# Kernel tuning notes

Hardware: AMD Instinct MI355X
Metric: run time of the kernel (lower is better)

The kernel has to match this reference:

```python
import jax, jax.numpy as jnp
import numpy as np

B, C, H, W = 4, 512, 64, 64
CQ = C // 8  # 64 channels for each of query/key projections


def conv1x1(t, w, b):
    # t: [B, Cin, H, W], w: [Cout, Cin], b: [Cout]
    return jnp.einsum('bchw,oc->bohw', t, w) + b[None, :, None, None]


def setup_inputs() -> dict:
    key = jax.random.key(0)
    ks = jax.random.split(key, 12)
    s = 0.05
    return {
        'x':   jax.random.normal(ks[0], (B, C, H, W), jnp.float32),
        'dep': jax.random.normal(ks[1], (B, C, H, W), jnp.float32),
        'wq':  jax.random.normal(ks[2], (CQ, C), jnp.float32) * s,
        'bq':  jnp.zeros((CQ,), jnp.float32),
        'wqd': jax.random.normal(ks[3], (CQ, C), jnp.float32) * s,
        'bqd': jnp.zeros((CQ,), jnp.float32),
        'wk':  jax.random.normal(ks[4], (CQ, C), jnp.float32) * s,
        'bk':  jnp.zeros((CQ,), jnp.float32),
        'wkd': jax.random.normal(ks[5], (CQ, C), jnp.float32) * s,
        'bkd': jnp.zeros((CQ,), jnp.float32),
        'wv':  jax.random.normal(ks[6], (C, C), jnp.float32) * s,
        'bv':  jnp.zeros((C,), jnp.float32),
        'gamma': jnp.full((1,), 0.5, jnp.float32),
    }


def reference(x, dep, wq, bq, wqd, bqd, wk, bk, wkd, bkd, wv, bv, gamma):
    b, c, h, w = x.shape
    n = h * w
    # concatenated RGB+depth query/key projections: [B, 2*CQ, N]
    q = jnp.concatenate([conv1x1(x, wq, bq), conv1x1(dep, wqd, bqd)], axis=1).reshape(b, -1, n)
    k = jnp.concatenate([conv1x1(x, wk, bk), conv1x1(dep, wkd, bkd)], axis=1).reshape(b, -1, n)
    # energy[b, i, j] = sum_d q[b, d, i] * k[b, d, j]  -> [B, N, N]
    energy = jnp.einsum('bdi,bdj->bij', q, k)
    attn = jax.nn.softmax(energy, axis=-1)
    v = conv1x1(x, wv, bv).reshape(b, c, n)  # [B, C, N]
    # out[b, c, i] = sum_j v[b, c, j] * attn[b, i, j]
    out = jnp.einsum('bcj,bij->bci', v, attn).reshape(b, c, h, w)
    return gamma.reshape(()) * out + x
```

## Files before the change

### kernel.cpp

```cpp
#include <hip/hip_runtime.h>


typedef __attribute__((ext_vector_type(8))) short bf16x8;
typedef __attribute__((ext_vector_type(4))) float f32x4;

__device__ __forceinline__ float bf2f(unsigned short u) {
  return __builtin_bit_cast(float, (unsigned int)u << 16);
}
__device__ __forceinline__ unsigned short f2bf(float f) {
  unsigned int u = __builtin_bit_cast(unsigned int, f);
  u = u + 0x7fffu + ((u >> 16) & 1u);
  return (unsigned short)(u >> 16);
}
__device__ __forceinline__ float bflo(unsigned int u) {
  return __builtin_bit_cast(float, u << 16);
}

__device__ __forceinline__ void gld16(const char* g, char* l) {
  __builtin_amdgcn_global_load_lds(
      (const __attribute__((address_space(1))) unsigned int*)g,
      (__attribute__((address_space(3))) unsigned int*)l, 16, 0, 0);
}

__device__ __forceinline__ int detect_fp32_mode(const void* xv) {
  const unsigned int* p = (const unsigned int*)xv;
  const int lane = threadIdx.x & 63;
  const unsigned int w0 = p[lane];
  const unsigned int w1 = p[64 + lane];
  int cnt = 0;
  const unsigned short us[4] = {
      (unsigned short)(w0 & 0xffffu), (unsigned short)(w0 >> 16),
      (unsigned short)(w1 & 0xffffu), (unsigned short)(w1 >> 16)};
#pragma unroll
  for (int h = 0; h < 4; ++h) {
    const float a = fabsf(bf2f(us[h]));
    cnt += (a > 9.0e-13f && a < 32.0f) ? 1 : 0;
  }
#pragma unroll
  for (int mm = 32; mm >= 1; mm >>= 1) cnt += __shfl_xor(cnt, mm, 64);
  return cnt < 220;
}

__global__ __launch_bounds__(256) void prep_kernel(
    const void* wq, const void* bq, const void* wqd, const void* bqd,
    const void* wk, const void* bk, const void* wkd, const void* bkd,
    const void* wv, const void* bv, const void* gam, const void* x,
    unsigned short* __restrict__ Whi, unsigned short* __restrict__ Wlo,
    float* __restrict__ Bcat, float* __restrict__ gamF)
{
  const int fp32mode = detect_fp32_mode(x);
  const int row = blockIdx.x;
  const void* src; const void* bsrc; int srow;
  if (row < 64)       { src = wq;  bsrc = bq;  srow = row; }
  else if (row < 128) { src = wqd; bsrc = bqd; srow = row - 64; }
  else if (row < 192) { src = wk;  bsrc = bk;  srow = row - 128; }
  else if (row < 256) { src = wkd; bsrc = bkd; srow = row - 192; }
  else                { src = wv;  bsrc = bv;  srow = row - 256; }
  for (int c = threadIdx.x; c < 512; c += 256) {
    const float v = fp32mode ? ((const float*)src)[(size_t)srow * 512 + c]
                             : bf2f(((const unsigned short*)src)[(size_t)srow * 512 + c]);
    const unsigned short h = f2bf(v);
    Whi[(size_t)row * 512 + c] = h;
    Wlo[(size_t)row * 512 + c] = f2bf(v - bf2f(h));
  }
  if (threadIdx.x == 0) {
    Bcat[row] = fp32mode ? ((const float*)bsrc)[srow]
                         : bf2f(((const unsigned short*)bsrc)[srow]);
    if (row == 0)
      gamF[0] = fp32mode ? ((const float*)gam)[0]
                         : bf2f(((const unsigned short*)gam)[0]);
  }
}

__device__ __forceinline__ void stage_X(
    const void* __restrict__ src, int fp32mode, int b, int n0,
    int cbase, int nn,
    unsigned short* __restrict__ Xhi, unsigned short* __restrict__ Xlo)
{
  float v0a[16], v1a[16];
  if (fp32mode) {
    const float* s = (const float*)src;
#pragma unroll
    for (int r = 0; r < 16; ++r) {
      const int c = cbase + r * 32;
      const float2 f2 = *(const float2*)(s + (((size_t)b * 512 + c) << 12) + n0 + nn);
      v0a[r] = f2.x; v1a[r] = f2.y;
    }
  } else {
    const unsigned short* s = (const unsigned short*)src;
#pragma unroll
    for (int r = 0; r < 16; ++r) {
      const int c = cbase + r * 32;
      const unsigned int v2 =
          *(const unsigned int*)(s + (((size_t)b * 512 + c) << 12) + n0 + nn);
      v0a[r] = bflo(v2 & 0xffffu); v1a[r] = bflo(v2 >> 16);
    }
  }
#pragma unroll
  for (int r = 0; r < 16; ++r) {
    const int c = cbase + r * 32;
    const unsigned short h0 = f2bf(v0a[r]), h1 = f2bf(v1a[r]);
    Xhi[nn * 522 + c]       = h0;
    Xhi[(nn + 1) * 522 + c] = h1;
    Xlo[nn * 522 + c]       = f2bf(v0a[r] - bf2f(h0));
    Xlo[(nn + 1) * 522 + c] = f2bf(v1a[r] - bf2f(h1));
  }
}

__device__ __forceinline__ void do_tile2(
    const unsigned short* __restrict__ Whi, const unsigned short* __restrict__ Wlo,
    const float* bsh,
    const unsigned short* Xhi, const unsigned short* Xlo, int fp32mode,
    int wrow0, int kind, int d0,
    int l15, int quad,
    char* __restrict__ QT, char* __restrict__ KT, char* __restrict__ VT)
{
  bf16x8 wh[16], wl[16];
  {
    const unsigned short* whi = Whi + (size_t)(wrow0 + l15) * 512 + quad * 8;
#pragma unroll
    for (int ks = 0; ks < 16; ++ks)
      wh[ks] = *(const bf16x8*)(whi + ks * 32);
    if (fp32mode) {
      const unsigned short* wlo = Wlo + (size_t)(wrow0 + l15) * 512 + quad * 8;
#pragma unroll
      for (int ks = 0; ks < 16; ++ks)
        wl[ks] = *(const bf16x8*)(wlo + ks * 32);
    }
  }
  f32x4 A0, A1, B0, B1, C0, C1;
#pragma unroll
  for (int r = 0; r < 4; ++r) {
    A0[r] = A1[r] = bsh[wrow0 + quad * 4 + r];
    B0[r] = B1[r] = C0[r] = C1[r] = 0.f;
  }
  const unsigned short* x0h = Xhi + l15 * 522;
  const unsigned short* x1h = Xhi + (16 + l15) * 522;
  const unsigned short* x0l = Xlo + l15 * 522;
  const unsigned short* x1l = Xlo + (16 + l15) * 522;
#pragma unroll
  for (int ks = 0; ks < 16; ++ks) {
    const int o = ks * 32 + quad * 8;
    const bf16x8 b0 = *(const bf16x8*)(x0h + o);
    const bf16x8 b1 = *(const bf16x8*)(x1h + o);
    A0 = __builtin_amdgcn_mfma_f32_16x16x32_bf16(wh[ks], b0, A0, 0, 0, 0);
    A1 = __builtin_amdgcn_mfma_f32_16x16x32_bf16(wh[ks], b1, A1, 0, 0, 0);
    if (fp32mode) {
      const bf16x8 c0 = *(const bf16x8*)(x0l + o);
      const bf16x8 c1 = *(const bf16x8*)(x1l + o);
      B0 = __builtin_amdgcn_mfma_f32_16x16x32_bf16(wh[ks], c0, B0, 0, 0, 0);
      C0 = __builtin_amdgcn_mfma_f32_16x16x32_bf16(wl[ks], b0, C0, 0, 0, 0);
      B1 = __builtin_amdgcn_mfma_f32_16x16x32_bf16(wh[ks], c1, B1, 0, 0, 0);
      C1 = __builtin_amdgcn_mfma_f32_16x16x32_bf16(wl[ks], b1, C1, 0, 0, 0);
    }
  }
  const f32x4 a0 = fp32mode ? (A0 + B0) + C0 : A0;
  const f32x4 a1 = fp32mode ? (A1 + B1) + C1 : A1;
#pragma unroll
  for (int ns = 0; ns < 2; ++ns) {
    const f32x4 acc = ns ? a1 : a0;
    const int n = ns * 16 + l15;
    if (kind <= 1) {
      ushort4 h, l;
#pragma unroll
      for (int r = 0; r < 4; ++r) {
        const float f = acc[r];
        const unsigned short hh = f2bf(f);
        ((unsigned short*)&h)[r] = hh;
        ((unsigned short*)&l)[r] = f2bf(f - bf2f(hh));
      }
      const unsigned lin = (unsigned)(n * 256 + (d0 + quad * 4) * 2);
      if (kind == 0) {
        *(ushort4*)(QT + lin) = h;
        *(ushort4*)(QT + 8192 + lin) = l;
      } else {
        const unsigned off = lin ^ ((unsigned)(n & 7) << 4);
        *(ushort4*)(KT + off) = h;
        *(ushort4*)(KT + 8192 + off) = l;
      }
    } else {
#pragma unroll
      for (int r = 0; r < 4; ++r) {
        const int c = d0 + quad * 4 + r;
        const unsigned off =
            ((unsigned)(c * 64 + n * 2)) ^ ((unsigned)(c & 7) << 4);
        *(unsigned short*)(VT + off) = f2bf(acc[r]);
      }
    }
  }
}

__global__ __launch_bounds__(512, 2) void proj_kernel(
    const void* __restrict__ x, const void* __restrict__ dep,
    const unsigned short* __restrict__ Whi, const unsigned short* __restrict__ Wlo,
    const float* __restrict__ Bcat,
    unsigned short* __restrict__ Qhi, unsigned short* __restrict__ Qlo,
    unsigned short* __restrict__ Kst, unsigned short* __restrict__ Vst)
{
  __shared__ unsigned short Xhi[32 * 522];
  __shared__ unsigned short Xlo[32 * 522];
  __shared__ char QT[16384];
  __shared__ char KT[16384];
  __shared__ char VT[32768];
  __shared__ float bsh[768];
  const int fp32mode = detect_fp32_mode(x);
  const int tid  = threadIdx.x;
  const int lane = tid & 63;
  const int w    = tid >> 6;
  const int l15  = lane & 15;
  const int quad = lane >> 4;
  const int b  = blockIdx.y;
  const int t  = blockIdx.x;
  const int n0 = t * 32;

  const int cbase = tid >> 4;
  const int nn    = (tid & 15) * 2;

  for (int i = tid; i < 768; i += 512) bsh[i] = Bcat[i];

  stage_X(x, fp32mode, b, n0, cbase, nn, Xhi, Xlo);
  __syncthreads();

  for (int rt = w; rt < 40; rt += 8) {
    if (rt < 4)
      do_tile2(Whi, Wlo, bsh, Xhi, Xlo, fp32mode, rt * 16,             0, rt * 16,
               l15, quad, QT, KT, VT);
    else if (rt < 8)
      do_tile2(Whi, Wlo, bsh, Xhi, Xlo, fp32mode, 128 + (rt - 4) * 16, 1, (rt - 4) * 16,
               l15, quad, QT, KT, VT);
    else
      do_tile2(Whi, Wlo, bsh, Xhi, Xlo, fp32mode, 256 + (rt - 8) * 16, 2, (rt - 8) * 16,
               l15, quad, QT, KT, VT);
  }
  __syncthreads();

  {
    char* vdst = (char*)Vst + (((size_t)b * 128 + t) << 15);
#pragma unroll
    for (int i = 0; i < 4; ++i) {
      const int off = i * 8192 + tid * 16;
      *(uint4*)(vdst + off) = *(const uint4*)(VT + off);
    }
  }
  stage_X(dep, fp32mode, b, n0, cbase, nn, Xhi, Xlo);
  __syncthreads();

  {
    const int rt = w;
    if (rt < 4)
      do_tile2(Whi, Wlo, bsh, Xhi, Xlo, fp32mode, 64 + rt * 16,        0, 64 + rt * 16,
               l15, quad, QT, KT, VT);
    else
      do_tile2(Whi, Wlo, bsh, Xhi, Xlo, fp32mode, 192 + (rt - 4) * 16, 1, 64 + (rt - 4) * 16,
               l15, quad, QT, KT, VT);
  }
  __syncthreads();

  {
    char* kdst = (char*)Kst + (((size_t)b * 128 + t) << 14);
#pragma unroll
    for (int i = 0; i < 2; ++i) {
      const int off = i * 8192 + tid * 16;
      *(uint4*)(kdst + off) = *(const uint4*)(KT + off);
    }
    const size_t qoff = ((((size_t)b << 12) + n0) * 128) * 2;
    *(uint4*)((char*)Qhi + qoff + tid * 16) = *(const uint4*)(QT + tid * 16);
    *(uint4*)((char*)Qlo + qoff + tid * 16) = *(const uint4*)(QT + 8192 + tid * 16);
  }
}

__global__ __launch_bounds__(768, 3) void attn_kernel(
    const unsigned short* __restrict__ Qhi, const unsigned short* __restrict__ Qlo,
    const unsigned short* __restrict__ Kst, const unsigned short* __restrict__ Vst,
    const void* __restrict__ x, const float* __restrict__ gamF,
    void* __restrict__ outp)
{
  __shared__ char KL[2][16384];
  __shared__ char VL[2][32768];
  __shared__ unsigned short P[2][64][40];
  __shared__ float lstat[2][4][16];

  const int fp32mode = detect_fp32_mode(x);
  const int tid  = threadIdx.x;
  const int lane = tid & 63;
  const int w    = tid >> 6;
  const int l15  = lane & 15;
  const int quad = lane >> 4;
  const int id   = blockIdx.x;
  const int b    = (id >> 1) & 3;
  const int n0   = (((id >> 3) << 1) | (id & 1)) * 64;

  asm volatile("" :: "v"(fp32mode) : "memory");

  const char* Kb = (const char*)Kst + (((size_t)b * 128) << 14);
  const char* Vb = (const char*)Vst + (((size_t)b * 128) << 15);

  if (w < 4) {
    const int ihE = w >> 1;
    const int jt  = w & 1;
    bf16x8 qh[2][4], ql[2][4];
#pragma unroll
    for (int itq = 0; itq < 2; ++itq) {
      const size_t qb =
          (((size_t)b << 12) + n0 + ihE * 32 + itq * 16 + l15) * 128 + quad * 8;
#pragma unroll
      for (int ds = 0; ds < 4; ++ds) {
        qh[itq][ds] = *(const bf16x8*)(Qhi + qb + ds * 32);
        ql[itq][ds] = *(const bf16x8*)(Qlo + qb + ds * 32);
      }
    }
#pragma unroll
    for (int ch = 0; ch < 4; ++ch) {
      const int c = w + ch * 4;
      gld16(Kb + c * 1024 + lane * 16, &KL[0][c * 1024]);
    }
    float lpart[2] = {0.f, 0.f};

    for (int t = 0; t <= 128; ++t) {
      asm volatile("s_waitcnt vmcnt(0) lgkmcnt(0)" ::: "memory");
      __builtin_amdgcn_sched_barrier(0);
      __builtin_amdgcn_s_barrier();
      __builtin_amdgcn_sched_barrier(0);
      if (t < 128) {
        const int cur = t & 1;
        if (t < 127) {
          const char* src = Kb + ((size_t)(t + 1) << 14);
#pragma unroll
          for (int ch = 0; ch < 4; ++ch) {
            const int c = w + ch * 4;
            gld16(src + c * 1024 + lane * 16, &KL[cur ^ 1][c * 1024]);
          }
        }
        __builtin_amdgcn_sched_barrier(0);
        const int row = jt * 16 + l15;
        const unsigned rsw = (unsigned)(row & 7) << 4;
        const char* kb = &KL[cur][0];
        bf16x8 kh[4], kl[4];
#pragma unroll
        for (int ds = 0; ds < 4; ++ds) {
          const unsigned off = ((unsigned)(row * 256 + quad * 16 + ds * 64)) ^ rsw;
          kh[ds] = *(const bf16x8*)(kb + off);
          kl[ds] = *(const bf16x8*)(kb + 8192 + off);
        }
        f32x4 ea[2], eb[2], ec[2];
#pragma unroll
        for (int itq = 0; itq < 2; ++itq) {
          ea[itq] = (f32x4){0.f, 0.f, 0.f, 0.f};
          eb[itq] = (f32x4){0.f, 0.f, 0.f, 0.f};
          ec[itq] = (f32x4){0.f, 0.f, 0.f, 0.f};
        }
        __builtin_amdgcn_s_setprio(1);
#pragma unroll
        for (int ds = 0; ds < 4; ++ds)
#pragma unroll
          for (int itq = 0; itq < 2; ++itq) {
            ea[itq] = __builtin_amdgcn_mfma_f32_16x16x32_bf16(kh[ds], qh[itq][ds], ea[itq], 0, 0, 0);
            eb[itq] = __builtin_amdgcn_mfma_f32_16x16x32_bf16(kh[ds], ql[itq][ds], eb[itq], 0, 0, 0);
            ec[itq] = __builtin_amdgcn_mfma_f32_16x16x32_bf16(kl[ds], qh[itq][ds], ec[itq], 0, 0, 0);
          }
        __builtin_amdgcn_s_setprio(0);
#pragma unroll
        for (int itq = 0; itq < 2; ++itq) {
          const f32x4 e = (ea[itq] + eb[itq]) + ec[itq];
          const float p0 = __expf(e[0] - 32.0f);
          const float p1 = __expf(e[1] - 32.0f);
          const float p2 = __expf(e[2] - 32.0f);
          const float p3 = __expf(e[3] - 32.0f);
          const unsigned short u0 = f2bf(p0), u1 = f2bf(p1);
          const unsigned short u2 = f2bf(p2), u3 = f2bf(p3);
          lpart[itq] += (bf2f(u0) + bf2f(u1)) + (bf2f(u2) + bf2f(u3));
          unsigned int* dst = (unsigned int*)
              (&P[cur][ihE * 32 + itq * 16 + l15][jt * 16 + quad * 4]);
          dst[0] = (unsigned int)u0 | ((unsigned int)u1 << 16);
          dst[1] = (unsigned int)u2 | ((unsigned int)u3 << 16);
        }
      }
    }
#pragma unroll
    for (int itq = 0; itq < 2; ++itq) {
      float lp = lpart[itq];
      lp += __shfl_xor(lp, 16, 64);
      lp += __shfl_xor(lp, 32, 64);
      if (quad == 0) lstat[jt][ihE * 2 + itq][l15] = lp;
    }
    __syncthreads();
    return;
  }

  const int wv = w - 4;
#pragma unroll
  for (int k = 0; k < 4; ++k) {
    const int c = wv * 4 + k;
    gld16(Vb + c * 1024 + lane * 16, &VL[0][c * 1024]);
  }
  f32x4 acc[4][4];
#pragma unroll
  for (int ct = 0; ct < 4; ++ct)
#pragma unroll
    for (int itv = 0; itv < 4; ++itv) acc[ct][itv] = (f32x4){0.f, 0.f, 0.f, 0.f};

  for (int t = 0; t <= 128; ++t) {
    if (t <= 127)
      asm volatile("s_waitcnt vmcnt(4)" ::: "memory");
    else
      asm volatile("s_waitcnt vmcnt(0)" ::: "memory");
    __builtin_amdgcn_sched_barrier(0);
    __builtin_amdgcn_s_barrier();
    __builtin_amdgcn_sched_barrier(0);
    if (t >= 1) {
      const int pb = (t - 1) & 1;
      bf16x8 pf[4];
#pragma unroll
      for (int itv = 0; itv < 4; ++itv)
        pf[itv] = *(const bf16x8*)(&P[pb][itv * 16 + l15][quad * 8]);
      const char* vb = &VL[pb][0];
      __builtin_amdgcn_s_setprio(1);
#pragma unroll
      for (int ct = 0; ct < 4; ++ct) {
        const int c = wv * 64 + ct * 16 + l15;
        const unsigned off =
            ((unsigned)(c * 64 + quad * 16)) ^ ((unsigned)(c & 7) << 4);
        const bf16x8 va = *(const bf16x8*)(vb + off);
#pragma unroll
        for (int itv = 0; itv < 4; ++itv)
          acc[ct][itv] = __builtin_amdgcn_mfma_f32_16x16x32_bf16(va, pf[itv], acc[ct][itv], 0, 0, 0);
      }
      __builtin_amdgcn_s_setprio(0);
      __builtin_amdgcn_sched_barrier(0);
    }
    if (t < 127) {
      const char* src = Vb + ((size_t)(t + 1) << 15);
#pragma unroll
      for (int k = 0; k < 4; ++k) {
        const int c = wv * 4 + k;
        gld16(src + c * 1024 + lane * 16, &VL[(t + 1) & 1][c * 1024]);
      }
    }
  }
  __syncthreads();

  const float gv = gamF[0];
  float sc[4];
#pragma unroll
  for (int itv = 0; itv < 4; ++itv) {
    const float l = lstat[0][itv][l15] + lstat[1][itv][l15];
    sc[itv] = gv / l;
  }
#pragma unroll
  for (int ct = 0; ct < 4; ++ct)
#pragma unroll
    for (int r = 0; r < 4; ++r) {
      const int c_g = wv * 64 + ct * 16 + quad * 4 + r;
      const size_t brow = ((size_t)b * 512 + c_g) << 12;
#pragma unroll
      for (int itv = 0; itv < 4; ++itv) {
        const size_t addr = brow + n0 + itv * 16 + l15;
        const float o = sc[itv] * acc[ct][itv][r];
        if (fp32mode) {
          ((float*)outp)[addr] = o + ((const float*)x)[addr];
        } else {
          ((unsigned short*)outp)[addr] =
              f2bf(o + bf2f(((const unsigned short*)x)[addr]));
        }
      }
    }
}

extern "C" void kernel_launch(void* const* d_in, const int* in_sizes, int n_in,
                              void* d_out, int out_size, void* d_ws, size_t ws_size,
                              hipStream_t stream) {
  const void* x    = d_in[0];
  const void* dep  = d_in[1];
  const void* wq   = d_in[2];
  const void* bq   = d_in[3];
  const void* wqd  = d_in[4];
  const void* bqd  = d_in[5];
  const void* wk   = d_in[6];
  const void* bk   = d_in[7];
  const void* wkd  = d_in[8];
  const void* bkd  = d_in[9];
  const void* wv   = d_in[10];
  const void* bv   = d_in[11];
  const void* gam  = d_in[12];

  unsigned short* Whi = (unsigned short*)d_ws;
  unsigned short* Wlo = Whi + (size_t)768 * 512;
  float* Bcat = (float*)(Wlo + (size_t)768 * 512);
  float* gamF = Bcat + 768;
  unsigned short* Qhi = (unsigned short*)((char*)d_ws + ((size_t)2 << 20));
  unsigned short* Qlo = (unsigned short*)((char*)d_ws + ((size_t)6 << 20));
  unsigned short* Kst = (unsigned short*)((char*)d_ws + ((size_t)10 << 20));
  unsigned short* Vst = (unsigned short*)((char*)d_ws + ((size_t)18 << 20));

  prep_kernel<<<768, 256, 0, stream>>>(wq, bq, wqd, bqd, wk, bk, wkd, bkd,
                                       wv, bv, gam, x, Whi, Wlo, Bcat, gamF);
  proj_kernel<<<dim3(128, 4), 512, 0, stream>>>(x, dep, Whi, Wlo, Bcat,
                                                Qhi, Qlo, Kst, Vst);
  attn_kernel<<<256, 768, 0, stream>>>(Qhi, Qlo, Kst, Vst, x, gamF, d_out);
}
```

Before: 442.4 us.

## Double-buffer weight loads in projection tile and widen X staging loads

Result: no change. 436.3 us (-1.4%).

```diff
diff --git a/kernel.cpp b/kernel.cpp
--- a/kernel.cpp
+++ b/kernel.cpp
@@ -77,33 +77,35 @@
     int cbase, int nn,
     unsigned short* __restrict__ Xhi, unsigned short* __restrict__ Xlo)
 {
-  float v0a[16], v1a[16];
+  float v[8][4];
   if (fp32mode) {
     const float* s = (const float*)src;
 #pragma unroll
-    for (int r = 0; r < 16; ++r) {
-      const int c = cbase + r * 32;
-      const float2 f2 = *(const float2*)(s + (((size_t)b * 512 + c) << 12) + n0 + nn);
-      v0a[r] = f2.x; v1a[r] = f2.y;
+    for (int r = 0; r < 8; ++r) {
+      const int c = cbase + r * 64;
+      const float4 f4 = *(const float4*)(s + (((size_t)b * 512 + c) << 12) + n0 + nn);
+      v[r][0] = f4.x; v[r][1] = f4.y; v[r][2] = f4.z; v[r][3] = f4.w;
     }
   } else {
     const unsigned short* s = (const unsigned short*)src;
 #pragma unroll
-    for (int r = 0; r < 16; ++r) {
-      const int c = cbase + r * 32;
-      const unsigned int v2 =
-          *(const unsigned int*)(s + (((size_t)b * 512 + c) << 12) + n0 + nn);
-      v0a[r] = bflo(v2 & 0xffffu); v1a[r] = bflo(v2 >> 16);
-    }
-  }
-#pragma unroll
-  for (int r = 0; r < 16; ++r) {
-    const int c = cbase + r * 32;
-    const unsigned short h0 = f2bf(v0a[r]), h1 = f2bf(v1a[r]);
-    Xhi[nn * 522 + c]       = h0;
-    Xhi[(nn + 1) * 522 + c] = h1;
-    Xlo[nn * 522 + c]       = f2bf(v0a[r] - bf2f(h0));
-    Xlo[(nn + 1) * 522 + c] = f2bf(v1a[r] - bf2f(h1));
+    for (int r = 0; r < 8; ++r) {
+      const int c = cbase + r * 64;
+      const uint2 u2 = *(const uint2*)(s + (((size_t)b * 512 + c) << 12) + n0 + nn);
+      v[r][0] = bflo(u2.x & 0xffffu); v[r][1] = bflo(u2.x >> 16);
+      v[r][2] = bflo(u2.y & 0xffffu); v[r][3] = bflo(u2.y >> 16);
+    }
+  }
+  __builtin_amdgcn_sched_barrier(0);
+#pragma unroll
+  for (int r = 0; r < 8; ++r) {
+    const int c = cbase + r * 64;
+#pragma unroll
+    for (int k = 0; k < 4; ++k) {
+      const unsigned short h = f2bf(v[r][k]);
+      Xhi[(nn + k) * 522 + c] = h;
+      Xlo[(nn + k) * 522 + c] = f2bf(v[r][k] - bf2f(h));
+    }
   }
 }
 
@@ -115,45 +117,155 @@
     int l15, int quad,
     char* __restrict__ QT, char* __restrict__ KT, char* __restrict__ VT)
 {
-  bf16x8 wh[16], wl[16];
-  {
-    const unsigned short* whi = Whi + (size_t)(wrow0 + l15) * 512 + quad * 8;
-#pragma unroll
-    for (int ks = 0; ks < 16; ++ks)
-      wh[ks] = *(const bf16x8*)(whi + ks * 32);
-    if (fp32mode) {
-      const unsigned short* wlo = Wlo + (size_t)(wrow0 + l15) * 512 + quad * 8;
-#pragma unroll
-      for (int ks = 0; ks < 16; ++ks)
-        wl[ks] = *(const bf16x8*)(wlo + ks * 32);
-    }
-  }
   f32x4 A0, A1, B0, B1, C0, C1;
 #pragma unroll
   for (int r = 0; r < 4; ++r) {
     A0[r] = A1[r] = bsh[wrow0 + quad * 4 + r];
     B0[r] = B1[r] = C0[r] = C1[r] = 0.f;
   }
+  const unsigned short* whi = Whi + (size_t)(wrow0 + l15) * 512 + quad * 8;
+  const unsigned short* wlo = Wlo + (size_t)(wrow0 + l15) * 512 + quad * 8;
   const unsigned short* x0h = Xhi + l15 * 522;
   const unsigned short* x1h = Xhi + (16 + l15) * 522;
   const unsigned short* x0l = Xlo + l15 * 522;
   const unsigned short* x1l = Xlo + (16 + l15) * 522;
-#pragma unroll
-  for (int ks = 0; ks < 16; ++ks) {
-    const int o = ks * 32 + quad * 8;
-    const bf16x8 b0 = *(const bf16x8*)(x0h + o);
-    const bf16x8 b1 = *(const bf16x8*)(x1h + o);
-    A0 = __builtin_amdgcn_mfma_f32_16x16x32_bf16(wh[ks], b0, A0, 0, 0, 0);
-    A1 = __builtin_amdgcn_mfma_f32_16x16x32_bf16(wh[ks], b1, A1, 0, 0, 0);
-    if (fp32mode) {
+
+  if (fp32mode) {
+    bf16x8 h0[4], l0[4], h1[4], l1[4];
+#pragma unroll
+    for (int j = 0; j < 4; ++j) {
+      h0[j] = *(const bf16x8*)(whi + j * 32);
+      l0[j] = *(const bf16x8*)(wlo + j * 32);
+    }
+#pragma unroll
+    for (int j = 0; j < 4; ++j) {
+      h1[j] = *(const bf16x8*)(whi + (4 + j) * 32);
+      l1[j] = *(const bf16x8*)(wlo + (4 + j) * 32);
+    }
+    __builtin_amdgcn_sched_barrier(0);
+    asm volatile("s_waitcnt vmcnt(8)" ::: "memory");
+    __builtin_amdgcn_sched_barrier(0);
+#pragma unroll
+    for (int j = 0; j < 4; ++j) {
+      const int o = j * 32 + quad * 8;
+      const bf16x8 b0 = *(const bf16x8*)(x0h + o);
+      const bf16x8 b1 = *(const bf16x8*)(x1h + o);
       const bf16x8 c0 = *(const bf16x8*)(x0l + o);
       const bf16x8 c1 = *(const bf16x8*)(x1l + o);
-      B0 = __builtin_amdgcn_mfma_f32_16x16x32_bf16(wh[ks], c0, B0, 0, 0, 0);
-      C0 = __builtin_amdgcn_mfma_f32_16x16x32_bf16(wl[ks], b0, C0, 0, 0, 0);
-      B1 = __builtin_amdgcn_mfma_f32_16x16x32_bf16(wh[ks], c1, B1, 0, 0, 0);
-      C1 = __builtin_amdgcn_mfma_f32_16x16x32_bf16(wl[ks], b1, C1, 0, 0, 0);
-    }
-  }
+      A0 = __builtin_amdgcn_mfma_f32_16x16x32_bf16(h0[j], b0, A0, 0, 0, 0);
+      A1 = __builtin_amdgcn_mfma_f32_16x16x32_bf16(h0[j], b1, A1, 0, 0, 0);
+      B0 = __builtin_amdgcn_mfma_f32_16x16x32_bf16(h0[j], c0, B0, 0, 0, 0);
+      C0 = __builtin_amdgcn_mfma_f32_16x16x32_bf16(l0[j], b0, C0, 0, 0, 0);
+      B1 = __builtin_amdgcn_mfma_f32_16x16x32_bf16(h0[j], c1, B1, 0, 0, 0);
+      C1 = __builtin_amdgcn_mfma_f32_16x16x32_bf16(l0[j], b1, C1, 0, 0, 0);
+    }
+#pragma unroll
+    for (int j = 0; j < 4; ++j) {
+      h0[j] = *(const bf16x8*)(whi + (8 + j) * 32);
+      l0[j] = *(const bf16x8*)(wlo + (8 + j) * 32);
+    }
+    __builtin_amdgcn_sched_barrier(0);
+    asm volatile("s_waitcnt vmcnt(8)" ::: "memory");
+    __builtin_amdgcn_sched_barrier(0);
+#pragma unroll
+    for (int j = 0; j < 4; ++j) {
+      const int o = (4 + j) * 32 + quad * 8;
+      const bf16x8 b0 = *(const bf16x8*)(x0h + o);
+      const bf16x8 b1 = *(const bf16x8*)(x1h + o);
+      const bf16x8 c0 = *(const bf16x8*)(x0l + o);
+      const bf16x8 c1 = *(const bf16x8*)(x1l + o);
+      A0 = __builtin_amdgcn_mfma_f32_16x16x32_bf16(h1[j], b0, A0, 0, 0, 0);
+      A1 = __builtin_amdgcn_mfma_f32_16x16x32_bf16(h1[j], b1, A1, 0, 0, 0);
+      B0 = __builtin_amdgcn_mfma_f32_16x16x32_bf16(h1[j], c0, B0, 0, 0, 0);
+      C0 = __builtin_amdgcn_mfma_f32_16x16x32_bf16(l1[j], b0, C0, 0, 0, 0);
+      B1 = __builtin_amdgcn_mfma_f32_16x16x32_bf16(h1[j], c1, B1, 0, 0, 0);
+      C1 = __builtin_amdgcn_mfma_f32_16x16x32_bf16(l1[j], b1, C1, 0, 0, 0);
+    }
+#pragma unroll
+    for (int j = 0; j < 4; ++j) {
+      h1[j] = *(const bf16x8*)(whi + (12 + j) * 32);
+      l1[j] = *(const bf16x8*)(wlo + (12 + j) * 32);
+    }
+    __builtin_amdgcn_sched_barrier(0);
+    asm volatile("s_waitcnt vmcnt(8)" ::: "memory");
+    __builtin_amdgcn_sched_barrier(0);
+#pragma unroll
+    for (int j = 0; j < 4; ++j) {
+      const int o = (8 + j) * 32 + quad * 8;
+      const bf16x8 b0 = *(const bf16x8*)(x0h + o);
+      const bf16x8 b1 = *(const bf16x8*)(x1h + o);
+      const bf16x8 c0 = *(const bf16x8*)(x0l + o);
+      const bf16x8 c1 = *(const bf16x8*)(x1l + o);
+      A0 = __builtin_amdgcn_mfma_f32_16x16x32_bf16(h0[j], b0, A0, 0, 0, 0);
+      A1 = __builtin_amdgcn_mfma_f32_16x16x32_bf16(h0[j], b1, A1, 0, 0, 0);
+      B0 = __builtin_amdgcn_mfma_f32_16x16x32_bf16(h0[j], c0, B0, 0, 0, 0);
+      C0 = __builtin_amdgcn_mfma_f32_16x16x32_bf16(l0[j], b0, C0, 0, 0, 0);
+      B1 = __builtin_amdgcn_mfma_f32_16x16x32_bf16(h0[j], c1, B1, 0, 0, 0);
+      C1 = __builtin_amdgcn_mfma_f32_16x16x32_bf16(l0[j], b1, C1, 0, 0, 0);
+    }
+    asm volatile("s_waitcnt vmcnt(0)" ::: "memory");
+    __builtin_amdgcn_sched_barrier(0);
+#pragma unroll
+    for (int j = 0; j < 4; ++j) {
+      const int o = (12 + j) * 32 + quad * 8;
+      const bf16x8 b0 = *(const bf16x8*)(x0h + o);
+      const bf16x8 b1 = *(const bf16x8*)(x1h + o);
+      const bf16x8 c0 = *(const bf16x8*)(x0l + o);
+      const bf16x8 c1 = *(const bf16x8*)(x1l + o);
+      A0 = __builtin_amdgcn_mfma_f32_16x16x32_bf16(h1[j], b0, A0, 0, 0, 0);
+      A1 = __builtin_amdgcn_mfma_f32_16x16x32_bf16(h1[j], b1, A1, 0, 0, 0);
+      B0 = __builtin_amdgcn_mfma_f32_16x16x32_bf16(h1[j], c0, B0, 0, 0, 0);
+      C0 = __builtin_amdgcn_mfma_f32_16x16x32_bf16(l1[j], b0, C0, 0, 0, 0);
+      B1 = __builtin_amdgcn_mfma_f32_16x16x32_bf16(h1[j], c1, B1, 0, 0, 0);
+      C1 = __builtin_amdgcn_mfma_f32_16x16x32_bf16(l1[j], b1, C1, 0, 0, 0);
+    }
+  } else {
+    bf16x8 h0[4], h1[4];
+#pragma unroll
+    for (int j = 0; j < 4; ++j) h0[j] = *(const bf16x8*)(whi + j * 32);
+#pragma unroll
+    for (int j = 0; j < 4; ++j) h1[j] = *(const bf16x8*)(whi + (4 + j) * 32);
+    __builtin_amdgcn_sched_barrier(0);
+    asm volatile("s_waitcnt vmcnt(4)" ::: "memory");
+    __builtin_amdgcn_sched_barrier(0);
+#pragma unroll
+    for (int j = 0; j < 4; ++j) {
+      const int o = j * 32 + quad * 8;
+      A0 = __builtin_amdgcn_mfma_f32_16x16x32_bf16(h0[j], *(const bf16x8*)(x0h + o), A0, 0, 0, 0);
+      A1 = __builtin_amdgcn_mfma_f32_16x16x32_bf16(h0[j], *(const bf16x8*)(x1h + o), A1, 0, 0, 0);
+    }
+#pragma unroll
+    for (int j = 0; j < 4; ++j) h0[j] = *(const bf16x8*)(whi + (8 + j) * 32);
+    __builtin_amdgcn_sched_barrier(0);
+    asm volatile("s_waitcnt vmcnt(4)" ::: "memory");
+    __builtin_amdgcn_sched_barrier(0);
+#pragma unroll
+    for (int j = 0; j < 4; ++j) {
+      const int o = (4 + j) * 32 + quad * 8;
+      A0 = __builtin_amdgcn_mfma_f32_16x16x32_bf16(h1[j], *(const bf16x8*)(x0h + o), A0, 0, 0, 0);
+      A1 = __builtin_amdgcn_mfma_f32_16x16x32_bf16(h1[j], *(const bf16x8*)(x1h + o), A1, 0, 0, 0);
+    }
+#pragma unroll
+    for (int j = 0; j < 4; ++j) h1[j] = *(const bf16x8*)(whi + (12 + j) * 32);
+    __builtin_amdgcn_sched_barrier(0);
+    asm volatile("s_waitcnt vmcnt(4)" ::: "memory");
+    __builtin_amdgcn_sched_barrier(0);
+#pragma unroll
+    for (int j = 0; j < 4; ++j) {
+      const int o = (8 + j) * 32 + quad * 8;
+      A0 = __builtin_amdgcn_mfma_f32_16x16x32_bf16(h0[j], *(const bf16x8*)(x0h + o), A0, 0, 0, 0);
+      A1 = __builtin_amdgcn_mfma_f32_16x16x32_bf16(h0[j], *(const bf16x8*)(x1h + o), A1, 0, 0, 0);
+    }
+    asm volatile("s_waitcnt vmcnt(0)" ::: "memory");
+    __builtin_amdgcn_sched_barrier(0);
+#pragma unroll
+    for (int j = 0; j < 4; ++j) {
+      const int o = (12 + j) * 32 + quad * 8;
+      A0 = __builtin_amdgcn_mfma_f32_16x16x32_bf16(h1[j], *(const bf16x8*)(x0h + o), A0, 0, 0, 0);
+      A1 = __builtin_amdgcn_mfma_f32_16x16x32_bf16(h1[j], *(const bf16x8*)(x1h + o), A1, 0, 0, 0);
+    }
+  }
+
   const f32x4 a0 = fp32mode ? (A0 + B0) + C0 : A0;
   const f32x4 a1 = fp32mode ? (A1 + B1) + C1 : A1;
 #pragma unroll
@@ -213,8 +325,8 @@
   const int t  = blockIdx.x;
   const int n0 = t * 32;
 
-  const int cbase = tid >> 4;
-  const int nn    = (tid & 15) * 2;
+  const int cbase = tid >> 3;
+  const int nn    = (tid & 7) * 4;
 
   for (int i = tid; i < 768; i += 512) bsh[i] = Bcat[i];
 
```

## Stream weight fragments with prefetch and run proj blocks over two tiles each

Applied to the files above, without the earlier changes.

Result: no change. 436.2 us (-1.4%).

```diff
diff --git a/kernel.cpp b/kernel.cpp
--- a/kernel.cpp
+++ b/kernel.cpp
@@ -77,37 +77,39 @@
     int cbase, int nn,
     unsigned short* __restrict__ Xhi, unsigned short* __restrict__ Xlo)
 {
-  float v0a[16], v1a[16];
+  float v[8][4];
   if (fp32mode) {
     const float* s = (const float*)src;
 #pragma unroll
-    for (int r = 0; r < 16; ++r) {
-      const int c = cbase + r * 32;
-      const float2 f2 = *(const float2*)(s + (((size_t)b * 512 + c) << 12) + n0 + nn);
-      v0a[r] = f2.x; v1a[r] = f2.y;
+    for (int r = 0; r < 8; ++r) {
+      const int c = cbase + r * 64;
+      const float4 f4 = *(const float4*)(s + (((size_t)b * 512 + c) << 12) + n0 + nn);
+      v[r][0] = f4.x; v[r][1] = f4.y; v[r][2] = f4.z; v[r][3] = f4.w;
     }
   } else {
     const unsigned short* s = (const unsigned short*)src;
 #pragma unroll
-    for (int r = 0; r < 16; ++r) {
-      const int c = cbase + r * 32;
-      const unsigned int v2 =
-          *(const unsigned int*)(s + (((size_t)b * 512 + c) << 12) + n0 + nn);
-      v0a[r] = bflo(v2 & 0xffffu); v1a[r] = bflo(v2 >> 16);
-    }
-  }
-#pragma unroll
-  for (int r = 0; r < 16; ++r) {
-    const int c = cbase + r * 32;
-    const unsigned short h0 = f2bf(v0a[r]), h1 = f2bf(v1a[r]);
-    Xhi[nn * 522 + c]       = h0;
-    Xhi[(nn + 1) * 522 + c] = h1;
-    Xlo[nn * 522 + c]       = f2bf(v0a[r] - bf2f(h0));
-    Xlo[(nn + 1) * 522 + c] = f2bf(v1a[r] - bf2f(h1));
-  }
-}
-
-__device__ __forceinline__ void do_tile2(
+    for (int r = 0; r < 8; ++r) {
+      const int c = cbase + r * 64;
+      const uint2 u2 = *(const uint2*)(s + (((size_t)b * 512 + c) << 12) + n0 + nn);
+      v[r][0] = bflo(u2.x & 0xffffu); v[r][1] = bflo(u2.x >> 16);
+      v[r][2] = bflo(u2.y & 0xffffu); v[r][3] = bflo(u2.y >> 16);
+    }
+  }
+  __builtin_amdgcn_sched_barrier(0);
+#pragma unroll
+  for (int r = 0; r < 8; ++r) {
+    const int c = cbase + r * 64;
+#pragma unroll
+    for (int k = 0; k < 4; ++k) {
+      const unsigned short h = f2bf(v[r][k]);
+      Xhi[(nn + k) * 522 + c] = h;
+      Xlo[(nn + k) * 522 + c] = f2bf(v[r][k] - bf2f(h));
+    }
+  }
+}
+
+__device__ __forceinline__ void do_tile_c(
     const unsigned short* __restrict__ Whi, const unsigned short* __restrict__ Wlo,
     const float* bsh,
     const unsigned short* Xhi, const unsigned short* Xlo, int fp32mode,
@@ -115,45 +117,46 @@
     int l15, int quad,
     char* __restrict__ QT, char* __restrict__ KT, char* __restrict__ VT)
 {
-  bf16x8 wh[16], wl[16];
-  {
-    const unsigned short* whi = Whi + (size_t)(wrow0 + l15) * 512 + quad * 8;
-#pragma unroll
-    for (int ks = 0; ks < 16; ++ks)
-      wh[ks] = *(const bf16x8*)(whi + ks * 32);
-    if (fp32mode) {
-      const unsigned short* wlo = Wlo + (size_t)(wrow0 + l15) * 512 + quad * 8;
-#pragma unroll
-      for (int ks = 0; ks < 16; ++ks)
-        wl[ks] = *(const bf16x8*)(wlo + ks * 32);
-    }
-  }
   f32x4 A0, A1, B0, B1, C0, C1;
 #pragma unroll
   for (int r = 0; r < 4; ++r) {
     A0[r] = A1[r] = bsh[wrow0 + quad * 4 + r];
     B0[r] = B1[r] = C0[r] = C1[r] = 0.f;
   }
-  const unsigned short* x0h = Xhi + l15 * 522;
-  const unsigned short* x1h = Xhi + (16 + l15) * 522;
-  const unsigned short* x0l = Xlo + l15 * 522;
-  const unsigned short* x1l = Xlo + (16 + l15) * 522;
-#pragma unroll
+  const unsigned short* wh_p = Whi + (size_t)(wrow0 + l15) * 512 + quad * 8;
+  const unsigned short* wl_p = Wlo + (size_t)(wrow0 + l15) * 512 + quad * 8;
+  const unsigned short* x0h = Xhi + l15 * 522 + quad * 8;
+  const unsigned short* x1h = Xhi + (16 + l15) * 522 + quad * 8;
+  const unsigned short* x0l = Xlo + l15 * 522 + quad * 8;
+  const unsigned short* x1l = Xlo + (16 + l15) * 522 + quad * 8;
+
+  bf16x8 hc = *(const bf16x8*)(wh_p);
+  bf16x8 lc;
+  if (fp32mode) lc = *(const bf16x8*)(wl_p);
+
+#pragma unroll 2
   for (int ks = 0; ks < 16; ++ks) {
-    const int o = ks * 32 + quad * 8;
+    bf16x8 hn, ln;
+    if (ks < 15) {
+      hn = *(const bf16x8*)(wh_p + (ks + 1) * 32);
+      if (fp32mode) ln = *(const bf16x8*)(wl_p + (ks + 1) * 32);
+    }
+    const int o = ks * 32;
     const bf16x8 b0 = *(const bf16x8*)(x0h + o);
     const bf16x8 b1 = *(const bf16x8*)(x1h + o);
-    A0 = __builtin_amdgcn_mfma_f32_16x16x32_bf16(wh[ks], b0, A0, 0, 0, 0);
-    A1 = __builtin_amdgcn_mfma_f32_16x16x32_bf16(wh[ks], b1, A1, 0, 0, 0);
+    A0 = __builtin_amdgcn_mfma_f32_16x16x32_bf16(hc, b0, A0, 0, 0, 0);
+    A1 = __builtin_amdgcn_mfma_f32_16x16x32_bf16(hc, b1, A1, 0, 0, 0);
     if (fp32mode) {
       const bf16x8 c0 = *(const bf16x8*)(x0l + o);
       const bf16x8 c1 = *(const bf16x8*)(x1l + o);
-      B0 = __builtin_amdgcn_mfma_f32_16x16x32_bf16(wh[ks], c0, B0, 0, 0, 0);
-      C0 = __builtin_amdgcn_mfma_f32_16x16x32_bf16(wl[ks], b0, C0, 0, 0, 0);
-      B1 = __builtin_amdgcn_mfma_f32_16x16x32_bf16(wh[ks], c1, B1, 0, 0, 0);
-      C1 = __builtin_amdgcn_mfma_f32_16x16x32_bf16(wl[ks], b1, C1, 0, 0, 0);
-    }
-  }
+      B0 = __builtin_amdgcn_mfma_f32_16x16x32_bf16(hc, c0, B0, 0, 0, 0);
+      C0 = __builtin_amdgcn_mfma_f32_16x16x32_bf16(lc, b0, C0, 0, 0, 0);
+      B1 = __builtin_amdgcn_mfma_f32_16x16x32_bf16(hc, c1, B1, 0, 0, 0);
+      C1 = __builtin_amdgcn_mfma_f32_16x16x32_bf16(lc, b1, C1, 0, 0, 0);
+    }
+    if (ks < 15) { hc = hn; if (fp32mode) lc = ln; }
+  }
+
   const f32x4 a0 = fp32mode ? (A0 + B0) + C0 : A0;
   const f32x4 a1 = fp32mode ? (A1 + B1) + C1 : A1;
 #pragma unroll
@@ -210,62 +213,62 @@
   const int l15  = lane & 15;
   const int quad = lane >> 4;
   const int b  = blockIdx.y;
-  const int t  = blockIdx.x;
-  const int n0 = t * 32;
-
-  const int cbase = tid >> 4;
-  const int nn    = (tid & 15) * 2;
+
+  const int cbase = tid >> 3;
+  const int nn    = (tid & 7) * 4;
 
   for (int i = tid; i < 768; i += 512) bsh[i] = Bcat[i];
 
-  stage_X(x, fp32mode, b, n0, cbase, nn, Xhi, Xlo);
-  __syncthreads();
-
-  for (int rt = w; rt < 40; rt += 8) {
-    if (rt < 4)
-      do_tile2(Whi, Wlo, bsh, Xhi, Xlo, fp32mode, rt * 16,             0, rt * 16,
-               l15, quad, QT, KT, VT);
-    else if (rt < 8)
-      do_tile2(Whi, Wlo, bsh, Xhi, Xlo, fp32mode, 128 + (rt - 4) * 16, 1, (rt - 4) * 16,
-               l15, quad, QT, KT, VT);
-    else
-      do_tile2(Whi, Wlo, bsh, Xhi, Xlo, fp32mode, 256 + (rt - 8) * 16, 2, (rt - 8) * 16,
-               l15, quad, QT, KT, VT);
-  }
-  __syncthreads();
-
-  {
-    char* vdst = (char*)Vst + (((size_t)b * 128 + t) << 15);
-#pragma unroll
-    for (int i = 0; i < 4; ++i) {
-      const int off = i * 8192 + tid * 16;
-      *(uint4*)(vdst + off) = *(const uint4*)(VT + off);
-    }
-  }
-  stage_X(dep, fp32mode, b, n0, cbase, nn, Xhi, Xlo);
-  __syncthreads();
-
-  {
-    const int rt = w;
-    if (rt < 4)
-      do_tile2(Whi, Wlo, bsh, Xhi, Xlo, fp32mode, 64 + rt * 16,        0, 64 + rt * 16,
-               l15, quad, QT, KT, VT);
-    else
-      do_tile2(Whi, Wlo, bsh, Xhi, Xlo, fp32mode, 192 + (rt - 4) * 16, 1, 64 + (rt - 4) * 16,
-               l15, quad, QT, KT, VT);
-  }
-  __syncthreads();
-
-  {
-    char* kdst = (char*)Kst + (((size_t)b * 128 + t) << 14);
-#pragma unroll
-    for (int i = 0; i < 2; ++i) {
-      const int off = i * 8192 + tid * 16;
-      *(uint4*)(kdst + off) = *(const uint4*)(KT + off);
-    }
-    const size_t qoff = ((((size_t)b << 12) + n0) * 128) * 2;
-    *(uint4*)((char*)Qhi + qoff + tid * 16) = *(const uint4*)(QT + tid * 16);
-    *(uint4*)((char*)Qlo + qoff + tid * 16) = *(const uint4*)(QT + 8192 + tid * 16);
+  for (int rep = 0; rep < 2; ++rep) {
+    const int t  = blockIdx.x + rep * 64;
+    const int n0 = t * 32;
+
+    stage_X(x, fp32mode, b, n0, cbase, nn, Xhi, Xlo);
+    __syncthreads();
+
+    for (int rt = w; rt < 40; rt += 8) {
+      int wrow0, kind, d0;
+      if (rt < 4)      { wrow0 = rt * 16;             kind = 0; d0 = rt * 16; }
+      else if (rt < 8) { wrow0 = 128 + (rt - 4) * 16; kind = 1; d0 = (rt - 4) * 16; }
+      else             { wrow0 = 256 + (rt - 8) * 16; kind = 2; d0 = (rt - 8) * 16; }
+      do_tile_c(Whi, Wlo, bsh, Xhi, Xlo, fp32mode, wrow0, kind, d0,
+                l15, quad, QT, KT, VT);
+    }
+    __syncthreads();
+
+    {
+      char* vdst = (char*)Vst + (((size_t)b * 128 + t) << 15);
+#pragma unroll
+      for (int i = 0; i < 4; ++i) {
+        const int off = i * 8192 + tid * 16;
+        *(uint4*)(vdst + off) = *(const uint4*)(VT + off);
+      }
+    }
+    stage_X(dep, fp32mode, b, n0, cbase, nn, Xhi, Xlo);
+    __syncthreads();
+
+    {
+      const int rt = w;
+      const int kind  = (rt < 4) ? 0 : 1;
+      const int wrow0 = (rt < 4) ? 64 + rt * 16 : 192 + (rt - 4) * 16;
+      const int d0    = 64 + (rt & 3) * 16;
+      do_tile_c(Whi, Wlo, bsh, Xhi, Xlo, fp32mode, wrow0, kind, d0,
+                l15, quad, QT, KT, VT);
+    }
+    __syncthreads();
+
+    {
+      char* kdst = (char*)Kst + (((size_t)b * 128 + t) << 14);
+#pragma unroll
+      for (int i = 0; i < 2; ++i) {
+        const int off = i * 8192 + tid * 16;
+        *(uint4*)(kdst + off) = *(const uint4*)(KT + off);
+      }
+      const size_t qoff = ((((size_t)b << 12) + n0) * 128) * 2;
+      *(uint4*)((char*)Qhi + qoff + tid * 16) = *(const uint4*)(QT + tid * 16);
+      *(uint4*)((char*)Qlo + qoff + tid * 16) = *(const uint4*)(QT + 8192 + tid * 16);
+    }
+    __syncthreads();
   }
 }
 
@@ -494,7 +497,7 @@
 
   prep_kernel<<<768, 256, 0, stream>>>(wq, bq, wqd, bqd, wk, bk, wkd, bkd,
                                        wv, bv, gam, x, Whi, Wlo, Bcat, gamF);
-  proj_kernel<<<dim3(128, 4), 512, 0, stream>>>(x, dep, Whi, Wlo, Bcat,
-                                                Qhi, Qlo, Kst, Vst);
+  proj_kernel<<<dim3(64, 4), 512, 0, stream>>>(x, dep, Whi, Wlo, Bcat,
+                                               Qhi, Qlo, Kst, Vst);
   attn_kernel<<<256, 768, 0, stream>>>(Qhi, Qlo, Kst, Vst, x, gamF, d_out);
 }
```
